# Kernel tuning notes

Hardware: AMD Instinct MI355X
Metric: run time of the kernel (lower is better)

## Reference

```python
import jax, jax.numpy as jnp
import numpy as np
import math

B, NQ, NK = 8, 1024, 2048
DQ = DK = DV = 1024
H = 8
DH = DV // H
EPS = 1e-5


def _layernorm(x, g, b):
    mu = jnp.mean(x, axis=-1, keepdims=True)
    var = jnp.mean(jnp.square(x - mu), axis=-1, keepdims=True)
    return (x - mu) * jax.lax.rsqrt(var + EPS) * g + b


def setup_inputs() -> dict:
    key = jax.random.key(0)
    ks = jax.random.split(key, 12)
    s_q = 1.0 / math.sqrt(DQ)
    s_v = 1.0 / math.sqrt(DV)
    return {
        "Q": jax.random.normal(ks[0], (B, NQ, DQ), jnp.float32),
        "K": jax.random.normal(ks[1], (B, NK, DK), jnp.float32),
        "Wq": jax.random.normal(ks[2], (DQ, DV), jnp.float32) * s_q,
        "bq": jnp.zeros((DV,), jnp.float32),
        "Wk": jax.random.normal(ks[3], (DK, DV), jnp.float32) * s_q,
        "bk": jnp.zeros((DV,), jnp.float32),
        "Wv": jax.random.normal(ks[4], (DK, DV), jnp.float32) * s_q,
        "bv": jnp.zeros((DV,), jnp.float32),
        "Wo": jax.random.normal(ks[5], (DV, DV), jnp.float32) * s_v,
        "bo": jnp.zeros((DV,), jnp.float32),
        "g0": jnp.ones((DV,), jnp.float32),
        "b0": jnp.zeros((DV,), jnp.float32),
        "g1": jnp.ones((DV,), jnp.float32),
        "b1": jnp.zeros((DV,), jnp.float32),
    }


def reference(Q, K, Wq, bq, Wk, bk, Wv, bv, Wo, bo, g0, b0, g1, b1):
    # projections
    q = Q @ Wq + bq                      # [B, NQ, DV]
    k = K @ Wk + bk                      # [B, NK, DV]
    v = K @ Wv + bv                      # [B, NK, DV]
    qh = q.reshape(B, NQ, H, DH)
    kh = k.reshape(B, NK, H, DH)
    vh = v.reshape(B, NK, H, DH)
    # NOTE: original scales by sqrt(dim_V), not sqrt(d_head)
    scale = 1.0 / math.sqrt(DV)
    logits = jnp.einsum("bqhd,bkhd->bhqk", qh, kh) * scale
    A = jax.nn.softmax(logits, axis=-1)
    # residual baked into attention output: Q_ + A @ V_
    Oh = qh + jnp.einsum("bhqk,bkhd->bqhd", A, vh)
    O = Oh.reshape(B, NQ, DV)
    O = _layernorm(O, g0, b0)
    O = O + jax.nn.relu(O @ Wo + bo)
    O = _layernorm(O, g1, b1)
    return O
```

## Files before the change

### kernel.cpp

```cpp
#include <hip/hip_runtime.h>
#include <stdint.h>

#define DEVI static __device__ __forceinline__

typedef __attribute__((ext_vector_type(8))) short short8;
typedef __attribute__((ext_vector_type(4))) float floatx4;
typedef __attribute__((ext_vector_type(4))) unsigned short ushortx4;

DEVI unsigned short f2bf(float f) {
  union { float f; uint32_t u; } v; v.f = f;
  uint32_t r = v.u + 0x7FFFu + ((v.u >> 16) & 1u);
  return (unsigned short)(r >> 16);
}
DEVI unsigned short f2bf_trunc(float f) {
  union { float f; uint32_t u; } v; v.f = f;
  return (unsigned short)(v.u >> 16);
}
DEVI float bf2f(unsigned short s) {
  union { uint32_t u; float f; } v; v.u = ((uint32_t)s) << 16;
  return v.f;
}
DEVI uint32_t fbits(float f) {
  union { float f; uint32_t u; } v; v.f = f;
  return v.u;
}
DEVI unsigned char f2fp8(float f) {
  return (unsigned char)(__builtin_amdgcn_cvt_pk_fp8_f32(f, f, 0, false) & 0xff);
}

DEVI void lds_cp16(void* lds, const void* g) {
  __builtin_amdgcn_global_load_lds(
      (const __attribute__((address_space(1))) uint32_t*)g,
      reinterpret_cast<__attribute__((address_space(3))) uint32_t*>(
          (uint32_t)reinterpret_cast<uintptr_t>(lds)),
      16, 0, 0);
}

__global__ __launch_bounds__(256) void cvt_qk(const float* __restrict__ Q,
                                              const float* __restrict__ K,
                                              unsigned short* __restrict__ Qb,
                                              unsigned char* __restrict__ Kf8) {
  const int bid = blockIdx.x;
  if (bid < 8192) {
    const size_t i = (size_t)bid * 256 + threadIdx.x;
    const floatx4 v = ((const floatx4*)Q)[i];
    ushortx4 o;
    o.x = f2bf(v.x); o.y = f2bf(v.y); o.z = f2bf(v.z); o.w = f2bf(v.w);
    ((ushortx4*)Qb)[i] = o;
  } else {
    const size_t i = (size_t)(bid - 8192) * 256 + threadIdx.x;
    const floatx4 v = ((const floatx4*)K)[i];
    int p = __builtin_amdgcn_cvt_pk_fp8_f32(v.x, v.y, 0, false);
    p = __builtin_amdgcn_cvt_pk_fp8_f32(v.z, v.w, p, true);
    ((int*)Kf8)[i] = p;
  }
}

__global__ __launch_bounds__(256) void wtrans4(const float* __restrict__ Wq,
                                               const float* __restrict__ Wk,
                                               const float* __restrict__ Wv,
                                               const float* __restrict__ Wo,
                                               unsigned short* __restrict__ Wt,
                                               unsigned char* __restrict__ Wt8) {
  __shared__ float t[32][33];
  const int tx = threadIdx.x, ty = threadIdx.y;
  const int z = blockIdx.z;
  const float* W = (z == 0) ? Wq : (z == 1) ? Wk : (z == 2) ? Wv : Wo;
  const int c0 = blockIdx.x * 32, r0 = blockIdx.y * 32;
#pragma unroll
  for (int i = 0; i < 4; i++)
    t[ty + i * 8][tx] = W[(size_t)(r0 + ty + i * 8) * 1024 + c0 + tx];
  __syncthreads();
  if (z == 0 || z == 3) {
    unsigned short* D = Wt + (z == 0 ? 0 : (size_t)1024 * 1024);
#pragma unroll
    for (int i = 0; i < 4; i++)
      D[(size_t)(c0 + ty + i * 8) * 1024 + r0 + tx] = f2bf(t[tx][ty + i * 8]);
  } else {
    unsigned char* D = Wt8 + (z == 1 ? 0 : (size_t)1024 * 1024);
#pragma unroll
    for (int i = 0; i < 4; i++)
      D[(size_t)(c0 + ty + i * 8) * 1024 + r0 + tx] = f2fp8(t[tx][ty + i * 8]);
  }
}

template <int EPI>
__global__ __launch_bounds__(256, 3) void gemm_bt(
    const unsigned short* __restrict__ A, const unsigned short* __restrict__ Bt,
    const float* __restrict__ bias, const unsigned short* __restrict__ X1,
    void* __restrict__ Cout) {
  __shared__ unsigned short As[2][4][128][8];
  __shared__ unsigned short Bs[2][4][128][8];

  const int tid = threadIdx.x;
  const int lane = tid & 63, w = tid >> 6;
  const int wr = w >> 1, wc = w & 1;
  const int qd = lane >> 4, l16 = lane & 15;
  const int bid = blockIdx.x;
  const int xcd = bid & 7, loc = bid >> 3;
  const int m0 = (xcd * 8 + (loc & 7)) * 128;
  const int n0 = (loc >> 3) * 128;

  floatx4 acc[4][4];
#pragma unroll
  for (int i = 0; i < 4; i++)
#pragma unroll
    for (int j = 0; j < 4; j++) { floatx4 z = {0.f, 0.f, 0.f, 0.f}; acc[i][j] = z; }

  const int prow = tid & 127;
  const unsigned short* aptr = A + (size_t)(m0 + prow) * 1024 + ((tid >> 7) << 3);
  const unsigned short* bptr = Bt + (size_t)(n0 + prow) * 1024 + ((tid >> 7) << 3);
  const int dstoff = tid * 8;

  lds_cp16(&As[0][0][0][0] + dstoff, aptr);
  lds_cp16(&As[0][0][0][0] + dstoff + 2048, aptr + 16);
  lds_cp16(&Bs[0][0][0][0] + dstoff, bptr);
  lds_cp16(&Bs[0][0][0][0] + dstoff + 2048, bptr + 16);

  for (int it = 0; it < 32; it++) {
    __syncthreads();
    if (it < 31) {
      const int nb = (it + 1) & 1, k0 = (it + 1) * 32;
      lds_cp16(&As[nb][0][0][0] + dstoff, aptr + k0);
      lds_cp16(&As[nb][0][0][0] + dstoff + 2048, aptr + k0 + 16);
      lds_cp16(&Bs[nb][0][0][0] + dstoff, bptr + k0);
      lds_cp16(&Bs[nb][0][0][0] + dstoff + 2048, bptr + k0 + 16);
    }
    const int cur = it & 1;
    short8 af[4], bf[4];
#pragma unroll
    for (int mi = 0; mi < 4; mi++)
      af[mi] = *(const short8*)&As[cur][qd][wr * 64 + mi * 16 + l16][0];
#pragma unroll
    for (int ni = 0; ni < 4; ni++)
      bf[ni] = *(const short8*)&Bs[cur][qd][wc * 64 + ni * 16 + l16][0];
#pragma unroll
    for (int mi = 0; mi < 4; mi++)
#pragma unroll
      for (int ni = 0; ni < 4; ni++)
        acc[mi][ni] =
            __builtin_amdgcn_mfma_f32_16x16x32_bf16(af[mi], bf[ni], acc[mi][ni], 0, 0, 0);
  }

#pragma unroll
  for (int mi = 0; mi < 4; mi++) {
#pragma unroll
    for (int ni = 0; ni < 4; ni++) {
      const int row = m0 + wr * 64 + mi * 16 + qd * 4;
      const int col = n0 + wc * 64 + ni * 16 + l16;
      const float bv = bias[col];
      if constexpr (EPI == 0) {
        unsigned short* C = (unsigned short*)Cout;
#pragma unroll
        for (int r = 0; r < 4; r++)
          C[(size_t)(row + r) * 1024 + col] = f2bf(acc[mi][ni][r] + bv);
      } else {
        float* C = (float*)Cout;
#pragma unroll
        for (int r = 0; r < 4; r++) {
          const float x1 = bf2f(X1[(size_t)(row + r) * 1024 + col]);
          C[(size_t)(row + r) * 1024 + col] = x1 + fmaxf(acc[mi][ni][r] + bv, 0.f);
        }
      }
    }
  }
}

__global__ __launch_bounds__(256, 3) void gemm_kv_f8(
    const unsigned char* __restrict__ A, const unsigned char* __restrict__ Bt,
    const float* __restrict__ biasK, const float* __restrict__ biasV,
    unsigned short* __restrict__ CK, unsigned char* __restrict__ CV8) {
  __shared__ unsigned char As[2][4][128][16];
  __shared__ unsigned char Bs[2][4][128][16];

  const int tid = threadIdx.x;
  const int lane = tid & 63, w = tid >> 6;
  const int wr = w >> 1, wc = w & 1;
  const int qd = lane >> 4, l16 = lane & 15;
  const int bid = blockIdx.x;
  const int xcd = bid & 7, loc = bid >> 3;
  const int m0 = (xcd * 16 + (loc & 15)) * 128;
  const int n0 = (loc >> 4) * 128;

  floatx4 acc[4][4];
#pragma unroll
  for (int i = 0; i < 4; i++)
#pragma unroll
    for (int j = 0; j < 4; j++) { floatx4 z = {0.f, 0.f, 0.f, 0.f}; acc[i][j] = z; }

  const int srow = tid & 127, sc = tid >> 7;
  const unsigned char* aptr = A + (size_t)(m0 + srow) * 1024 + sc * 16;
  const unsigned char* bptr = Bt + (size_t)(n0 + srow) * 1024 + sc * 16;
  unsigned char* dA = &As[0][sc][srow][0];
  unsigned char* dB = &Bs[0][sc][srow][0];

  lds_cp16(dA, aptr);
  lds_cp16(dA + 4096, aptr + 32);
  lds_cp16(dB, bptr);
  lds_cp16(dB + 4096, bptr + 32);

  for (int it = 0; it < 16; it++) {
    __syncthreads();
    if (it < 15) {
      const int nb = (it + 1) & 1, k0 = (it + 1) * 64;
      lds_cp16(dA + nb * 8192, aptr + k0);
      lds_cp16(dA + nb * 8192 + 4096, aptr + k0 + 32);
      lds_cp16(dB + nb * 8192, bptr + k0);
      lds_cp16(dB + nb * 8192 + 4096, bptr + k0 + 32);
    }
    const int cur = it & 1;
    const int coff = (qd & 1) * 8, chi = qd >> 1;
    long a8[4][2], b8[4][2];
#pragma unroll
    for (int mi = 0; mi < 4; mi++) {
      const int row = wr * 64 + mi * 16 + l16;
      a8[mi][0] = *(const long*)&As[cur][chi][row][coff];
      a8[mi][1] = *(const long*)&As[cur][2 + chi][row][coff];
    }
#pragma unroll
    for (int ni = 0; ni < 4; ni++) {
      const int row = wc * 64 + ni * 16 + l16;
      b8[ni][0] = *(const long*)&Bs[cur][chi][row][coff];
      b8[ni][1] = *(const long*)&Bs[cur][2 + chi][row][coff];
    }
#pragma unroll
    for (int mi = 0; mi < 4; mi++)
#pragma unroll
      for (int ni = 0; ni < 4; ni++)
        acc[mi][ni] = __builtin_amdgcn_mfma_f32_16x16x32_fp8_fp8(
            a8[mi][0], b8[ni][0], acc[mi][ni], 0, 0, 0);
#pragma unroll
    for (int mi = 0; mi < 4; mi++)
#pragma unroll
      for (int ni = 0; ni < 4; ni++)
        acc[mi][ni] = __builtin_amdgcn_mfma_f32_16x16x32_fp8_fp8(
            a8[mi][1], b8[ni][1], acc[mi][ni], 0, 0, 0);
  }

#pragma unroll
  for (int mi = 0; mi < 4; mi++) {
#pragma unroll
    for (int ni = 0; ni < 4; ni++) {
      const int row = m0 + wr * 64 + mi * 16 + qd * 4;
      const int col = n0 + wc * 64 + ni * 16 + l16;
      if (col < 1024) {
        const float bv = biasK[col];
#pragma unroll
        for (int r = 0; r < 4; r++)
          CK[(size_t)(row + r) * 1024 + col] = f2bf(acc[mi][ni][r] + bv);
      } else {
        const int vc = col - 1024;
        const float bv = biasV[vc];
        const int bb = row >> 11, nk = row & 2047;
        const int hh = vc >> 7, dh = vc & 127;
        int p = __builtin_amdgcn_cvt_pk_fp8_f32(acc[mi][ni][0] + bv,
                                                acc[mi][ni][1] + bv, 0, false);
        p = __builtin_amdgcn_cvt_pk_fp8_f32(acc[mi][ni][2] + bv,
                                            acc[mi][ni][3] + bv, p, true);
        *(uint32_t*)&CV8[((((size_t)(bb * 8 + hh)) * 256 + (nk >> 3)) * 128 + dh) * 8 +
                         (nk & 7)] = (uint32_t)p;
      }
    }
  }
}

__global__ __launch_bounds__(256, 3) void attn(
    const unsigned short* __restrict__ qb, const unsigned short* __restrict__ kb,
    const unsigned char* __restrict__ vt8, unsigned short* __restrict__ Ob) {
  __shared__ __align__(16) unsigned char smc[32768];
  unsigned short* sm16 = (unsigned short*)smc;

  const int tid = threadIdx.x;
  const int lane = tid & 63, w = tid >> 6;
  const int qd = lane >> 4, l16 = lane & 15;
  const int bid = blockIdx.x;
  const int qt = bid >> 6, bh = bid & 63;
  const int h = bh >> 3, b = bh & 7;
  const int m0 = qt * 128;

  const size_t qbase = ((size_t)(b * 1024 + m0)) * 1024 + h * 128;
  const size_t kbase = ((size_t)(b * 2048)) * 1024 + h * 128;
  const size_t vbase8 = (size_t)(b * 8 + h) * 262144;

#pragma unroll
  for (int i = 0; i < 8; i++) {
    const int p = i * 256 + tid;
    const int row = p & 127, c = p >> 7;
    lds_cp16(&sm16[c * 1024 + row * 8], qb + qbase + (size_t)row * 1024 + c * 8);
  }
  __syncthreads();
  short8 qf[2][4];
#pragma unroll
  for (int nt = 0; nt < 2; nt++)
#pragma unroll
    for (int ks = 0; ks < 4; ks++)
      qf[nt][ks] =
          *(const short8*)&sm16[(ks * 4 + qd) * 1024 + (w * 32 + nt * 16 + l16) * 8];
  __syncthreads();

#pragma unroll
  for (int i = 0; i < 2; i++) {
    const int p = i * 256 + tid;
    const int kr = p & 31, kc = p >> 5;
    lds_cp16(smc + kc * 512 + kr * 16, kb + kbase + (size_t)kr * 1024 + kc * 8);
  }
  {
    const int vc = tid >> 6, d2 = (tid & 63) * 2;
    lds_cp16(smc + 16384 + vc * 1024 + d2 * 8, vt8 + vbase8 + vc * 1024 + d2 * 8);
  }

  floatx4 oacc[8][2];
#pragma unroll
  for (int mt = 0; mt < 8; mt++)
#pragma unroll
    for (int nt = 0; nt < 2; nt++) { floatx4 z = {0.f, 0.f, 0.f, 0.f}; oacc[mt][nt] = z; }
  float lsum[2] = {0.f, 0.f};

  const int addrLo = ((qd & 1) * 32 + l16) * 4;
  const int addrHi = addrLo + 64;
  const bool loHalf = (lane < 32);

  for (int it = 0; it < 64; it++) {
    __syncthreads();
    if (it + 1 < 64) {
      const int nb = (it + 1) & 1, kv0 = (it + 1) * 32;
#pragma unroll
      for (int i = 0; i < 2; i++) {
        const int p = i * 256 + tid;
        const int kr = p & 31, kc = p >> 5;
        lds_cp16(smc + nb * 8192 + kc * 512 + kr * 16,
                 kb + kbase + (size_t)(kv0 + kr) * 1024 + kc * 8);
      }
      {
        const int vc = tid >> 6, d2 = (tid & 63) * 2;
        lds_cp16(smc + 16384 + nb * 4096 + vc * 1024 + d2 * 8,
                 vt8 + vbase8 + (size_t)kv0 * 128 + vc * 1024 + d2 * 8);
      }
    }
    const int cur = it & 1;

    floatx4 st[2][2];
#pragma unroll
    for (int mt = 0; mt < 2; mt++)
#pragma unroll
      for (int nt = 0; nt < 2; nt++) { floatx4 z = {0.f, 0.f, 0.f, 0.f}; st[mt][nt] = z; }
    __builtin_amdgcn_s_setprio(1);
#pragma unroll
    for (int ks = 0; ks < 4; ks++) {
      const short8 ka =
          *(const short8*)(smc + cur * 8192 + (ks * 4 + qd) * 512 + l16 * 16);
      const short8 kb2 =
          *(const short8*)(smc + cur * 8192 + (ks * 4 + qd) * 512 + (16 + l16) * 16);
#pragma unroll
      for (int nt = 0; nt < 2; nt++) {
        st[0][nt] = __builtin_amdgcn_mfma_f32_16x16x32_bf16(ka, qf[nt][ks], st[0][nt], 0, 0, 0);
        st[1][nt] = __builtin_amdgcn_mfma_f32_16x16x32_bf16(kb2, qf[nt][ks], st[1][nt], 0, 0, 0);
      }
    }
    __builtin_amdgcn_s_setprio(0);

    long vl[8];
#pragma unroll
    for (int mt = 0; mt < 8; mt++)
      vl[mt] = *(const long*)(smc + 16384 + cur * 4096 + qd * 1024 + (mt * 16 + l16) * 8);

    uint32_t pkf[2][2];
#pragma unroll
    for (int mt = 0; mt < 2; mt++)
#pragma unroll
      for (int nt = 0; nt < 2; nt++) {
        const float e0 = __expf(st[mt][nt][0] * 0.03125f);
        const float e1 = __expf(st[mt][nt][1] * 0.03125f);
        const float e2 = __expf(st[mt][nt][2] * 0.03125f);
        const float e3 = __expf(st[mt][nt][3] * 0.03125f);
        lsum[nt] += (e0 + e1) + (e2 + e3);
        int p = __builtin_amdgcn_cvt_pk_fp8_f32(e0, e1, 0, false);
        p = __builtin_amdgcn_cvt_pk_fp8_f32(e2, e3, p, true);
        pkf[mt][nt] = (uint32_t)p;
      }

#pragma unroll
    for (int nt = 0; nt < 2; nt++) {
      int lo0 = __builtin_amdgcn_ds_bpermute(addrLo, (int)pkf[0][nt]);
      int lo1 = __builtin_amdgcn_ds_bpermute(addrLo, (int)pkf[1][nt]);
      int hi0 = __builtin_amdgcn_ds_bpermute(addrHi, (int)pkf[0][nt]);
      int hi1 = __builtin_amdgcn_ds_bpermute(addrHi, (int)pkf[1][nt]);
      union { int i[2]; long l; } u;
      u.i[0] = loHalf ? lo0 : lo1;
      u.i[1] = loHalf ? hi0 : hi1;
      const long pfl = u.l;
      __builtin_amdgcn_s_setprio(1);
#pragma unroll
      for (int mt = 0; mt < 8; mt++)
        oacc[mt][nt] =
            __builtin_amdgcn_mfma_f32_16x16x32_fp8_fp8(vl[mt], pfl, oacc[mt][nt], 0, 0, 0);
      __builtin_amdgcn_s_setprio(0);
    }
  }

  float inv[2];
#pragma unroll
  for (int nt = 0; nt < 2; nt++) {
    float s = lsum[nt];
    s += __shfl_xor(s, 16);
    s += __shfl_xor(s, 32);
    inv[nt] = 1.f / s;
  }

  __syncthreads();
#pragma unroll
  for (int mt = 0; mt < 8; mt++)
#pragma unroll
    for (int nt = 0; nt < 2; nt++) {
      const int q = w * 32 + nt * 16 + l16;
#pragma unroll
      for (int r = 0; r < 4; r++) {
        const int dh = mt * 16 + qd * 4 + r;
        const int c = dh >> 3, off = dh & 7;
        sm16[q * 128 + ((c ^ (q & 15)) * 8) + off] = f2bf_trunc(oacc[mt][nt][r] * inv[nt]);
      }
    }
  __syncthreads();
#pragma unroll
  for (int i = 0; i < 8; i++) {
    const int p = i * 256 + tid;
    const int row = p >> 4, c = p & 15;
    const short8 ov = *(const short8*)&sm16[row * 128 + ((c ^ (row & 15)) * 8)];
    const short8 qres = *(const short8*)(qb + qbase + (size_t)row * 1024 + c * 8);
    union { unsigned short us[8]; short8 s; } o;
#pragma unroll
    for (int e = 0; e < 8; e++)
      o.us[e] = f2bf(bf2f((unsigned short)ov[e]) + bf2f((unsigned short)qres[e]));
    *(short8*)(Ob + qbase + (size_t)row * 1024 + c * 8) = o.s;
  }
}

__global__ __launch_bounds__(256) void ln_rows(const unsigned short* __restrict__ X,
                                               const float* __restrict__ g,
                                               const float* __restrict__ bb,
                                               unsigned short* __restrict__ Y) {
  __shared__ float red[8];
  const int row = blockIdx.x, tid = threadIdx.x;
  const int w = tid >> 6, lane = tid & 63;
  const ushortx4 u = ((const ushortx4*)(X + (size_t)row * 1024))[tid];
  float x0 = bf2f(u.x), x1 = bf2f(u.y), x2 = bf2f(u.z), x3 = bf2f(u.w);
  float s = x0 + x1 + x2 + x3;
  float s2 = x0 * x0 + x1 * x1 + x2 * x2 + x3 * x3;
#pragma unroll
  for (int off = 1; off < 64; off <<= 1) { s += __shfl_xor(s, off); s2 += __shfl_xor(s2, off); }
  if (lane == 0) { red[w] = s; red[4 + w] = s2; }
  __syncthreads();
  s = red[0] + red[1] + red[2] + red[3];
  s2 = red[4] + red[5] + red[6] + red[7];
  const float mu = s * (1.f / 1024.f);
  const float rs = rsqrtf(s2 * (1.f / 1024.f) - mu * mu + 1e-5f);
  const floatx4 gv = ((const floatx4*)g)[tid];
  const floatx4 bv = ((const floatx4*)bb)[tid];
  ushortx4 o;
  o.x = f2bf((x0 - mu) * rs * gv.x + bv.x);
  o.y = f2bf((x1 - mu) * rs * gv.y + bv.y);
  o.z = f2bf((x2 - mu) * rs * gv.z + bv.z);
  o.w = f2bf((x3 - mu) * rs * gv.w + bv.w);
  ((ushortx4*)(Y + (size_t)row * 1024))[tid] = o;
}

__global__ __launch_bounds__(256) void ln_f32(const float* __restrict__ X,
                                              const float* __restrict__ g,
                                              const float* __restrict__ bb,
                                              float* __restrict__ out) {
  __shared__ float red[8];
  const int row = blockIdx.x, tid = threadIdx.x;
  const int w = tid >> 6, lane = tid & 63;
  const floatx4 xv = ((const floatx4*)(X + (size_t)row * 1024))[tid];
  float x0 = xv.x, x1 = xv.y, x2 = xv.z, x3 = xv.w;
  float s = x0 + x1 + x2 + x3;
  float s2 = x0 * x0 + x1 * x1 + x2 * x2 + x3 * x3;
#pragma unroll
  for (int off = 1; off < 64; off <<= 1) { s += __shfl_xor(s, off); s2 += __shfl_xor(s2, off); }
  if (lane == 0) { red[w] = s; red[4 + w] = s2; }
  __syncthreads();
  s = red[0] + red[1] + red[2] + red[3];
  s2 = red[4] + red[5] + red[6] + red[7];
  const float mu = s * (1.f / 1024.f);
  const float rs = rsqrtf(s2 * (1.f / 1024.f) - mu * mu + 1e-5f);
  const floatx4 gv = ((const floatx4*)g)[tid];
  const floatx4 bv = ((const floatx4*)bb)[tid];
  floatx4 o;
  o.x = (x0 - mu) * rs * gv.x + bv.x;
  o.y = (x1 - mu) * rs * gv.y + bv.y;
  o.z = (x2 - mu) * rs * gv.z + bv.z;
  o.w = (x3 - mu) * rs * gv.w + bv.w;
  ((floatx4*)(out + (size_t)row * 1024))[tid] = o;
}

extern "C" void kernel_launch(void* const* d_in, const int* in_sizes, int n_in,
                              void* d_out, int out_size, void* d_ws, size_t ws_size,
                              hipStream_t stream) {
  (void)in_sizes; (void)n_in; (void)out_size; (void)ws_size;
  const float* Q  = (const float*)d_in[0];
  const float* K  = (const float*)d_in[1];
  const float* Wq = (const float*)d_in[2];
  const float* bq = (const float*)d_in[3];
  const float* Wk = (const float*)d_in[4];
  const float* bk = (const float*)d_in[5];
  const float* Wv = (const float*)d_in[6];
  const float* bv = (const float*)d_in[7];
  const float* Wo = (const float*)d_in[8];
  const float* bo = (const float*)d_in[9];
  const float* g0 = (const float*)d_in[10];
  const float* b0 = (const float*)d_in[11];
  const float* g1 = (const float*)d_in[12];
  const float* b1 = (const float*)d_in[13];
  float* out = (float*)d_out;

  char* ws = (char*)d_ws;
  const size_t MB = 1u << 20;
  unsigned short* Qb  = (unsigned short*)(ws + 0);
  unsigned short* X1  = (unsigned short*)(ws + 16 * MB);
  unsigned short* Wt  = (unsigned short*)(ws + 32 * MB);
  unsigned char*  Wt8 = (unsigned char*)(ws + 36 * MB);
  unsigned char*  Kf8 = (unsigned char*)(ws + 38 * MB);
  unsigned short* qbp = (unsigned short*)(ws + 54 * MB);
  unsigned short* kbp = (unsigned short*)(ws + 70 * MB);
  unsigned char*  vt8 = (unsigned char*)(ws + 102 * MB);
  unsigned short* O   = Qb;
  float* O2 = (float*)(ws + 70 * MB);

  unsigned short* Wqt = Wt;
  unsigned short* Wot = Wt + (size_t)1024 * 1024;

  cvt_qk<<<24576, 256, 0, stream>>>(Q, K, Qb, Kf8);
  wtrans4<<<dim3(32, 32, 4), dim3(32, 8), 0, stream>>>(Wq, Wk, Wv, Wo, Wt, Wt8);

  gemm_bt<0><<<512, 256, 0, stream>>>(Qb, Wqt, bq, nullptr, qbp);
  gemm_kv_f8<<<2048, 256, 0, stream>>>(Kf8, Wt8, bk, bv, kbp, vt8);
  attn<<<512, 256, 0, stream>>>(qbp, kbp, vt8, O);
  ln_rows<<<8192, 256, 0, stream>>>(O, g0, b0, X1);
  gemm_bt<2><<<512, 256, 0, stream>>>(X1, Wot, bo, X1, O2);
  ln_f32<<<8192, 256, 0, stream>>>(O2, g1, b1, out);
}
```

Baseline: 412.9 us.

## Double attention KV tile, widen fp8 LDS loads, store Wo output as bf16

The attention kernel now processes 64 keys per iteration instead of 32, using 48KB of LDS and a lower occupancy hint. This halves the number of barriers and loop iterations and gives more MFMA work per sync. The KV fp8 GEMM replaces two 8-byte LDS reads per fragment with one 16-byte read by reordering the k-chunk mapping. The output-projection epilogue now writes bf16 instead of fp32, and the final layernorm reads bf16, which halves that intermediate's traffic but adds rounding error before the last normalization.

After: 411.4 us. Within noise of the previous version (-0.4%).

```diff
diff --git a/kernel.cpp b/kernel.cpp
--- a/kernel.cpp
+++ b/kernel.cpp
@@ -6,6 +6,7 @@
 typedef __attribute__((ext_vector_type(8))) short short8;
 typedef __attribute__((ext_vector_type(4))) float floatx4;
 typedef __attribute__((ext_vector_type(4))) unsigned short ushortx4;
+typedef __attribute__((ext_vector_type(2))) long longx2;
 
 DEVI unsigned short f2bf(float f) {
   union { float f; uint32_t u; } v; v.f = f;
@@ -155,11 +156,11 @@
         for (int r = 0; r < 4; r++)
           C[(size_t)(row + r) * 1024 + col] = f2bf(acc[mi][ni][r] + bv);
       } else {
-        float* C = (float*)Cout;
+        unsigned short* C = (unsigned short*)Cout;
 #pragma unroll
         for (int r = 0; r < 4; r++) {
           const float x1 = bf2f(X1[(size_t)(row + r) * 1024 + col]);
-          C[(size_t)(row + r) * 1024 + col] = x1 + fmaxf(acc[mi][ni][r] + bv, 0.f);
+          C[(size_t)(row + r) * 1024 + col] = f2bf(x1 + fmaxf(acc[mi][ni][r] + bv, 0.f));
         }
       }
     }
@@ -209,32 +210,29 @@
       lds_cp16(dB + nb * 8192 + 4096, bptr + k0 + 32);
     }
     const int cur = it & 1;
-    const int coff = (qd & 1) * 8, chi = qd >> 1;
-    long a8[4][2], b8[4][2];
+    longx2 av[4], bvv[4];
 #pragma unroll
     for (int mi = 0; mi < 4; mi++) {
       const int row = wr * 64 + mi * 16 + l16;
-      a8[mi][0] = *(const long*)&As[cur][chi][row][coff];
-      a8[mi][1] = *(const long*)&As[cur][2 + chi][row][coff];
+      av[mi] = *(const longx2*)&As[cur][qd][row][0];
     }
 #pragma unroll
     for (int ni = 0; ni < 4; ni++) {
       const int row = wc * 64 + ni * 16 + l16;
-      b8[ni][0] = *(const long*)&Bs[cur][chi][row][coff];
-      b8[ni][1] = *(const long*)&Bs[cur][2 + chi][row][coff];
+      bvv[ni] = *(const longx2*)&Bs[cur][qd][row][0];
     }
 #pragma unroll
     for (int mi = 0; mi < 4; mi++)
 #pragma unroll
       for (int ni = 0; ni < 4; ni++)
         acc[mi][ni] = __builtin_amdgcn_mfma_f32_16x16x32_fp8_fp8(
-            a8[mi][0], b8[ni][0], acc[mi][ni], 0, 0, 0);
+            av[mi].x, bvv[ni].x, acc[mi][ni], 0, 0, 0);
 #pragma unroll
     for (int mi = 0; mi < 4; mi++)
 #pragma unroll
       for (int ni = 0; ni < 4; ni++)
         acc[mi][ni] = __builtin_amdgcn_mfma_f32_16x16x32_fp8_fp8(
-            a8[mi][1], b8[ni][1], acc[mi][ni], 0, 0, 0);
+            av[mi].y, bvv[ni].y, acc[mi][ni], 0, 0, 0);
   }
 
 #pragma unroll
@@ -264,10 +262,10 @@
   }
 }
 
-__global__ __launch_bounds__(256, 3) void attn(
+__global__ __launch_bounds__(256, 2) void attn(
     const unsigned short* __restrict__ qb, const unsigned short* __restrict__ kb,
     const unsigned char* __restrict__ vt8, unsigned short* __restrict__ Ob) {
-  __shared__ __align__(16) unsigned char smc[32768];
+  __shared__ __align__(16) unsigned char smc[49152];
   unsigned short* sm16 = (unsigned short*)smc;
 
   const int tid = threadIdx.x;
@@ -299,14 +297,16 @@
   __syncthreads();
 
 #pragma unroll
+  for (int i = 0; i < 4; i++) {
+    const int p = i * 256 + tid;
+    const int kr = p & 63, kc = p >> 6;
+    lds_cp16(smc + kc * 1024 + kr * 16, kb + kbase + (size_t)kr * 1024 + kc * 8);
+  }
+#pragma unroll
   for (int i = 0; i < 2; i++) {
     const int p = i * 256 + tid;
-    const int kr = p & 31, kc = p >> 5;
-    lds_cp16(smc + kc * 512 + kr * 16, kb + kbase + (size_t)kr * 1024 + kc * 8);
-  }
-  {
-    const int vc = tid >> 6, d2 = (tid & 63) * 2;
-    lds_cp16(smc + 16384 + vc * 1024 + d2 * 8, vt8 + vbase8 + vc * 1024 + d2 * 8);
+    const int d2 = (p & 63) * 2, vc = p >> 6;
+    lds_cp16(smc + 32768 + vc * 1024 + d2 * 8, vt8 + vbase8 + vc * 1024 + d2 * 8);
   }
 
   floatx4 oacc[8][2];
@@ -320,81 +320,88 @@
   const int addrHi = addrLo + 64;
   const bool loHalf = (lane < 32);
 
-  for (int it = 0; it < 64; it++) {
+  for (int it = 0; it < 32; it++) {
     __syncthreads();
-    if (it + 1 < 64) {
-      const int nb = (it + 1) & 1, kv0 = (it + 1) * 32;
+    if (it + 1 < 32) {
+      const int nb = (it + 1) & 1, kv0 = (it + 1) * 64;
+#pragma unroll
+      for (int i = 0; i < 4; i++) {
+        const int p = i * 256 + tid;
+        const int kr = p & 63, kc = p >> 6;
+        lds_cp16(smc + nb * 16384 + kc * 1024 + kr * 16,
+                 kb + kbase + (size_t)(kv0 + kr) * 1024 + kc * 8);
+      }
 #pragma unroll
       for (int i = 0; i < 2; i++) {
         const int p = i * 256 + tid;
-        const int kr = p & 31, kc = p >> 5;
-        lds_cp16(smc + nb * 8192 + kc * 512 + kr * 16,
-                 kb + kbase + (size_t)(kv0 + kr) * 1024 + kc * 8);
-      }
-      {
-        const int vc = tid >> 6, d2 = (tid & 63) * 2;
-        lds_cp16(smc + 16384 + nb * 4096 + vc * 1024 + d2 * 8,
+        const int d2 = (p & 63) * 2, vc = p >> 6;
+        lds_cp16(smc + 32768 + nb * 8192 + vc * 1024 + d2 * 8,
                  vt8 + vbase8 + (size_t)kv0 * 128 + vc * 1024 + d2 * 8);
       }
     }
     const int cur = it & 1;
 
-    floatx4 st[2][2];
-#pragma unroll
-    for (int mt = 0; mt < 2; mt++)
-#pragma unroll
-      for (int nt = 0; nt < 2; nt++) { floatx4 z = {0.f, 0.f, 0.f, 0.f}; st[mt][nt] = z; }
+    floatx4 st[4][2];
+#pragma unroll
+    for (int kt = 0; kt < 4; kt++)
+#pragma unroll
+      for (int nt = 0; nt < 2; nt++) { floatx4 z = {0.f, 0.f, 0.f, 0.f}; st[kt][nt] = z; }
     __builtin_amdgcn_s_setprio(1);
 #pragma unroll
     for (int ks = 0; ks < 4; ks++) {
-      const short8 ka =
-          *(const short8*)(smc + cur * 8192 + (ks * 4 + qd) * 512 + l16 * 16);
-      const short8 kb2 =
-          *(const short8*)(smc + cur * 8192 + (ks * 4 + qd) * 512 + (16 + l16) * 16);
+      short8 kf[4];
+#pragma unroll
+      for (int kt = 0; kt < 4; kt++)
+        kf[kt] = *(const short8*)(smc + cur * 16384 + (ks * 4 + qd) * 1024 +
+                                  (kt * 16 + l16) * 16);
+#pragma unroll
+      for (int kt = 0; kt < 4; kt++)
+#pragma unroll
+        for (int nt = 0; nt < 2; nt++)
+          st[kt][nt] =
+              __builtin_amdgcn_mfma_f32_16x16x32_bf16(kf[kt], qf[nt][ks], st[kt][nt], 0, 0, 0);
+    }
+    __builtin_amdgcn_s_setprio(0);
+
+    uint32_t pkf[4][2];
+#pragma unroll
+    for (int kt = 0; kt < 4; kt++)
 #pragma unroll
       for (int nt = 0; nt < 2; nt++) {
-        st[0][nt] = __builtin_amdgcn_mfma_f32_16x16x32_bf16(ka, qf[nt][ks], st[0][nt], 0, 0, 0);
-        st[1][nt] = __builtin_amdgcn_mfma_f32_16x16x32_bf16(kb2, qf[nt][ks], st[1][nt], 0, 0, 0);
-      }
-    }
-    __builtin_amdgcn_s_setprio(0);
-
-    long vl[8];
-#pragma unroll
-    for (int mt = 0; mt < 8; mt++)
-      vl[mt] = *(const long*)(smc + 16384 + cur * 4096 + qd * 1024 + (mt * 16 + l16) * 8);
-
-    uint32_t pkf[2][2];
-#pragma unroll
-    for (int mt = 0; mt < 2; mt++)
-#pragma unroll
-      for (int nt = 0; nt < 2; nt++) {
-        const float e0 = __expf(st[mt][nt][0] * 0.03125f);
-        const float e1 = __expf(st[mt][nt][1] * 0.03125f);
-        const float e2 = __expf(st[mt][nt][2] * 0.03125f);
-        const float e3 = __expf(st[mt][nt][3] * 0.03125f);
+        const float e0 = __expf(st[kt][nt][0] * 0.03125f);
+        const float e1 = __expf(st[kt][nt][1] * 0.03125f);
+        const float e2 = __expf(st[kt][nt][2] * 0.03125f);
+        const float e3 = __expf(st[kt][nt][3] * 0.03125f);
         lsum[nt] += (e0 + e1) + (e2 + e3);
         int p = __builtin_amdgcn_cvt_pk_fp8_f32(e0, e1, 0, false);
         p = __builtin_amdgcn_cvt_pk_fp8_f32(e2, e3, p, true);
-        pkf[mt][nt] = (uint32_t)p;
-      }
-
-#pragma unroll
-    for (int nt = 0; nt < 2; nt++) {
-      int lo0 = __builtin_amdgcn_ds_bpermute(addrLo, (int)pkf[0][nt]);
-      int lo1 = __builtin_amdgcn_ds_bpermute(addrLo, (int)pkf[1][nt]);
-      int hi0 = __builtin_amdgcn_ds_bpermute(addrHi, (int)pkf[0][nt]);
-      int hi1 = __builtin_amdgcn_ds_bpermute(addrHi, (int)pkf[1][nt]);
-      union { int i[2]; long l; } u;
-      u.i[0] = loHalf ? lo0 : lo1;
-      u.i[1] = loHalf ? hi0 : hi1;
-      const long pfl = u.l;
-      __builtin_amdgcn_s_setprio(1);
+        pkf[kt][nt] = (uint32_t)p;
+      }
+
+#pragma unroll
+    for (int s = 0; s < 2; s++) {
+      long vls[8];
 #pragma unroll
       for (int mt = 0; mt < 8; mt++)
-        oacc[mt][nt] =
-            __builtin_amdgcn_mfma_f32_16x16x32_fp8_fp8(vl[mt], pfl, oacc[mt][nt], 0, 0, 0);
-      __builtin_amdgcn_s_setprio(0);
+        vls[mt] = *(const long*)(smc + 32768 + cur * 8192 + (s * 4 + qd) * 1024 +
+                                 (mt * 16 + l16) * 8);
+#pragma unroll
+      for (int nt = 0; nt < 2; nt++) {
+        int lo0 = __builtin_amdgcn_ds_bpermute(addrLo, (int)pkf[2 * s][nt]);
+        int lo1 = __builtin_amdgcn_ds_bpermute(addrLo, (int)pkf[2 * s + 1][nt]);
+        int hi0 = __builtin_amdgcn_ds_bpermute(addrHi, (int)pkf[2 * s][nt]);
+        int hi1 = __builtin_amdgcn_ds_bpermute(addrHi, (int)pkf[2 * s + 1][nt]);
+        union { int i[2]; long l; } u;
+        u.i[0] = loHalf ? lo0 : lo1;
+        u.i[1] = loHalf ? hi0 : hi1;
+        const long pfl = u.l;
+        __builtin_amdgcn_s_setprio(1);
+#pragma unroll
+        for (int mt = 0; mt < 8; mt++)
+          oacc[mt][nt] =
+              __builtin_amdgcn_mfma_f32_16x16x32_fp8_fp8(vls[mt], pfl, oacc[mt][nt], 0, 0, 0);
+        __builtin_amdgcn_s_setprio(0);
+      }
     }
   }
 
@@ -464,15 +471,15 @@
   ((ushortx4*)(Y + (size_t)row * 1024))[tid] = o;
 }
 
-__global__ __launch_bounds__(256) void ln_f32(const float* __restrict__ X,
+__global__ __launch_bounds__(256) void ln_b2f(const unsigned short* __restrict__ X,
                                               const float* __restrict__ g,
                                               const float* __restrict__ bb,
                                               float* __restrict__ out) {
   __shared__ float red[8];
   const int row = blockIdx.x, tid = threadIdx.x;
   const int w = tid >> 6, lane = tid & 63;
-  const floatx4 xv = ((const floatx4*)(X + (size_t)row * 1024))[tid];
-  float x0 = xv.x, x1 = xv.y, x2 = xv.z, x3 = xv.w;
+  const ushortx4 u = ((const ushortx4*)(X + (size_t)row * 1024))[tid];
+  float x0 = bf2f(u.x), x1 = bf2f(u.y), x2 = bf2f(u.z), x3 = bf2f(u.w);
   float s = x0 + x1 + x2 + x3;
   float s2 = x0 * x0 + x1 * x1 + x2 * x2 + x3 * x3;
 #pragma unroll
@@ -524,7 +531,7 @@
   unsigned short* kbp = (unsigned short*)(ws + 70 * MB);
   unsigned char*  vt8 = (unsigned char*)(ws + 102 * MB);
   unsigned short* O   = Qb;
-  float* O2 = (float*)(ws + 70 * MB);
+  unsigned short* O2b = (unsigned short*)(ws + 70 * MB);
 
   unsigned short* Wqt = Wt;
   unsigned short* Wot = Wt + (size_t)1024 * 1024;
@@ -536,6 +543,6 @@
   gemm_kv_f8<<<2048, 256, 0, stream>>>(Kf8, Wt8, bk, bv, kbp, vt8);
   attn<<<512, 256, 0, stream>>>(qbp, kbp, vt8, O);
   ln_rows<<<8192, 256, 0, stream>>>(O, g0, b0, X1);
-  gemm_bt<2><<<512, 256, 0, stream>>>(X1, Wot, bo, X1, O2);
-  ln_f32<<<8192, 256, 0, stream>>>(O2, g1, b1, out);
-}
+  gemm_bt<2><<<512, 256, 0, stream>>>(X1, Wot, bo, X1, O2b);
+  ln_b2f<<<8192, 256, 0, stream>>>(O2b, g1, b1, out);
+}
```
